# Kernel tuning notes

Measured on AMD Instinct MI355X. Metric: run time of the kernel, lower is better.

The kernel has to match this reference:

```python
import jax, jax.numpy as jnp
import numpy as np

N = 50000
E = 640000
D = 128
H = 512
LN_EPS = 1e-5


def setup_inputs() -> dict:
    key = jax.random.key(0)
    ks = jax.random.split(key, 6)
    x = jax.random.normal(ks[0], (N, D), dtype=jnp.float32)
    edge_index = jax.random.randint(ks[1], (2, E), 0, N, dtype=jnp.int64)
    edge_dist = jax.random.uniform(ks[2], (E,), dtype=jnp.float32)
    # true out-degrees of src so degree normalization is realistic
    degrees = jax.ops.segment_sum(jnp.ones((E,), jnp.float32), edge_index[0], num_segments=N)
    W1 = jax.random.normal(ks[3], (2 * D + 2, H), dtype=jnp.float32) * (1.0 / np.sqrt(2 * D + 2))
    b1 = jnp.zeros((H,), jnp.float32)
    W2 = jax.random.normal(ks[4], (H, D), dtype=jnp.float32) * (1.0 / np.sqrt(H))
    b2 = jnp.zeros((D,), jnp.float32)
    gamma = jnp.ones((D,), jnp.float32)
    beta = jnp.zeros((D,), jnp.float32)
    return {"x": x, "W1": W1, "b1": b1, "W2": W2, "b2": b2,
            "gamma": gamma, "beta": beta,
            "edge_index": edge_index, "edge_dist": edge_dist, "degrees": degrees}


def reference(x, W1, b1, W2, b2, gamma, beta, edge_index, edge_dist, degrees):
    n = x.shape[0]
    src, dst = edge_index[0], edge_index[1]
    # gather neighbor features, scatter-add into source nodes
    msg = x[dst]                                             # [E, D]
    agg = jax.ops.segment_sum(msg, src, num_segments=n)      # [N, D]
    deg = jnp.maximum(degrees, 1.0)                          # clamp_min(1.0)
    agg = agg / deg[:, None]
    dist_sum = jax.ops.segment_sum(edge_dist, src, num_segments=n)  # [N]
    mean_dist = dist_sum / deg                               # [N]
    feat = jnp.concatenate([x, agg, degrees[:, None], mean_dist[:, None]], axis=-1)  # [N, 2D+2]
    h = jax.nn.relu(feat @ W1 + b1)
    out = h @ W2 + b2
    y = x + out
    mu = jnp.mean(y, axis=-1, keepdims=True)
    var = jnp.var(y, axis=-1, keepdims=True)
    return (y - mu) / jnp.sqrt(var + LN_EPS) * gamma + beta
```

## Files before the change

### kernel.cpp

```cpp
#include <hip/hip_runtime.h>
#include <hip/hip_bf16.h>

#define NN 50000
#define EE 640000
#define LN_EPS 1e-5f
#define KD 272
#define KB 544

typedef __bf16 bf16x8 __attribute__((ext_vector_type(8)));
typedef float f32x16 __attribute__((ext_vector_type(16)));

static __device__ __forceinline__ unsigned short f2bf(float f) {
    return __builtin_bit_cast(unsigned short, (__bf16)f);
}
static __device__ __forceinline__ float bflo(unsigned int u) {
    return __builtin_bit_cast(float, u << 16);
}
static __device__ __forceinline__ float bfhi(unsigned int u) {
    return __builtin_bit_cast(float, u & 0xffff0000u);
}

__global__ __launch_bounds__(256) void cast_x(const float* __restrict__ x,
                                              unsigned short* __restrict__ xbf) {
    int i = blockIdx.x * 256 + threadIdx.x;
    const float4* s = (const float4*)x + (size_t)i * 2;
    float4 a = s[0], b = s[1];
    unsigned short o[8] = { f2bf(a.x), f2bf(a.y), f2bf(a.z), f2bf(a.w),
                            f2bf(b.x), f2bf(b.y), f2bf(b.z), f2bf(b.w) };
    *(uint4*)(xbf + (size_t)i * 8) = *(const uint4*)o;
}

__global__ __launch_bounds__(256) void prep_weights(const float* __restrict__ W1,
                                                    const float* __restrict__ b1,
                                                    const float* __restrict__ W2,
                                                    unsigned short* __restrict__ W1Te,
                                                    unsigned short* __restrict__ W2T) {
    int b = blockIdx.x, tid = threadIdx.x;
    if (b < 512) {
        W1Te[(size_t)b * KD + tid] = f2bf(W1[(size_t)tid * 512 + b]);
        if (tid < 16) {
            float v = 0.f;
            if (tid == 0) v = W1[256 * 512 + b];
            else if (tid == 1) v = W1[257 * 512 + b];
            else if (tid == 2) v = b1[b];
            W1Te[(size_t)b * KD + 256 + tid] = f2bf(v);
        }
    } else {
        int c = b - 512;
        W2T[(size_t)c * 512 + tid]       = f2bf(W2[(size_t)tid * 128 + c]);
        W2T[(size_t)c * 512 + 256 + tid] = f2bf(W2[(size_t)(256 + tid) * 128 + c]);
    }
}

__global__ __launch_bounds__(256) void scanA(const float* __restrict__ degrees,
                                             int* __restrict__ blocksum) {
    __shared__ int wsum[4];
    int i = blockIdx.x * 256 + threadIdx.x;
    int v = (i < NN) ? (int)(degrees[i] + 0.5f) : 0;
    int s = v;
    for (int d = 1; d < 64; d <<= 1) s += __shfl_xor(s, d, 64);
    if ((threadIdx.x & 63) == 0) wsum[threadIdx.x >> 6] = s;
    __syncthreads();
    if (threadIdx.x == 0) blocksum[blockIdx.x] = wsum[0] + wsum[1] + wsum[2] + wsum[3];
}

__global__ __launch_bounds__(256) void scanB(const int* __restrict__ blocksum,
                                             int* __restrict__ blockoff, int nb) {
    __shared__ int wsum[4];
    int tid = threadIdx.x;
    int v = (tid < nb) ? blocksum[tid] : 0;
    int lane = tid & 63, wid = tid >> 6;
    int inc = v;
    for (int d = 1; d < 64; d <<= 1) { int t = __shfl_up(inc, d, 64); if (lane >= d) inc += t; }
    if (lane == 63) wsum[wid] = inc;
    __syncthreads();
    int add = 0;
    for (int w = 0; w < wid; w++) add += wsum[w];
    inc += add;
    if (tid < nb) blockoff[tid] = inc - v;
}

__global__ __launch_bounds__(256) void scanC(const float* __restrict__ degrees,
                                             const int* __restrict__ blockoff,
                                             int* __restrict__ start,
                                             int* __restrict__ cursor) {
    __shared__ int wsum[4];
    int tid = threadIdx.x;
    int i = blockIdx.x * 256 + tid;
    int v = (i < NN) ? (int)(degrees[i] + 0.5f) : 0;
    int lane = tid & 63, wid = tid >> 6;
    int inc = v;
    for (int d = 1; d < 64; d <<= 1) { int t = __shfl_up(inc, d, 64); if (lane >= d) inc += t; }
    if (lane == 63) wsum[wid] = inc;
    __syncthreads();
    int add = blockoff[blockIdx.x];
    for (int w = 0; w < wid; w++) add += wsum[w];
    int excl = add + inc - v;
    if (i < NN) { start[i] = excl; cursor[i] = excl; }
}

__global__ __launch_bounds__(256) void sort_kernel(const int* __restrict__ ei,
                                                   const float* __restrict__ edist,
                                                   int* __restrict__ cursor,
                                                   int* __restrict__ sorted_dst,
                                                   float* __restrict__ dist_sum) {
    int e = blockIdx.x * 256 + threadIdx.x;
    if (e >= EE) return;
    int s = ei[e];
    int d = ei[EE + e];
    int p = atomicAdd(cursor + s, 1);
    sorted_dst[p] = d;
    atomicAdd(dist_sum + s, edist[e]);
}

__global__ __launch_bounds__(256) void aggfeat_kernel(const unsigned short* __restrict__ xbf,
                                                      const int* __restrict__ start,
                                                      const float* __restrict__ degrees,
                                                      const int* __restrict__ sorted_dst,
                                                      const float* __restrict__ dist,
                                                      unsigned short* __restrict__ featbf) {
    int tid = threadIdx.x;
    int node = blockIdx.x * 4 + (tid >> 6);
    int lane = tid & 63;
    if (node >= NN) return;
    int st = start[node];
    int cnt = (int)(degrees[node] + 0.5f);
    float a0 = 0.f, a1 = 0.f;
    for (int base = 0; base < cnt; base += 64) {
        int rem = cnt - base;
        int nv = rem < 64 ? rem : 64;
        int didx = (lane < nv) ? sorted_dst[st + base + lane] : 0;
        int j = 0;
        for (; j + 4 <= nv; j += 4) {
            int d0 = __shfl(didx, j,     64);
            int d1 = __shfl(didx, j + 1, 64);
            int d2 = __shfl(didx, j + 2, 64);
            int d3 = __shfl(didx, j + 3, 64);
            unsigned int v0 = *(const unsigned int*)(xbf + (size_t)d0 * 128 + lane * 2);
            unsigned int v1 = *(const unsigned int*)(xbf + (size_t)d1 * 128 + lane * 2);
            unsigned int v2 = *(const unsigned int*)(xbf + (size_t)d2 * 128 + lane * 2);
            unsigned int v3 = *(const unsigned int*)(xbf + (size_t)d3 * 128 + lane * 2);
            a0 += bflo(v0) + bflo(v1) + bflo(v2) + bflo(v3);
            a1 += bfhi(v0) + bfhi(v1) + bfhi(v2) + bfhi(v3);
        }
        for (; j < nv; j++) {
            int dj = __shfl(didx, j, 64);
            unsigned int v = *(const unsigned int*)(xbf + (size_t)dj * 128 + lane * 2);
            a0 += bflo(v);
            a1 += bfhi(v);
        }
    }
    float degc = fmaxf(degrees[node], 1.0f);
    float inv = 1.0f / degc;
    unsigned short* row = featbf + (size_t)node * KD;
    *(unsigned int*)(row + lane * 2) = *(const unsigned int*)(xbf + (size_t)node * 128 + lane * 2);
    unsigned short o2[2] = { f2bf(a0 * inv), f2bf(a1 * inv) };
    *(unsigned int*)(row + 128 + lane * 2) = *(const unsigned int*)o2;
    if (lane < 4) {
        unsigned short t4[4] = { 0, 0, 0, 0 };
        if (lane == 0) { t4[0] = f2bf(degrees[node]); t4[1] = f2bf(dist[node] * inv); t4[2] = f2bf(1.0f); }
        *(uint2*)(row + 256 + lane * 4) = *(const uint2*)t4;
    }
}

__global__ __launch_bounds__(256, 2) void fused_mlp_ln(const unsigned short* __restrict__ featbf,
                                                       const unsigned short* __restrict__ W1Te,
                                                       const unsigned short* __restrict__ W2T,
                                                       const float* __restrict__ x,
                                                       const float* __restrict__ b2,
                                                       const float* __restrict__ gamma,
                                                       const float* __restrict__ beta,
                                                       float* __restrict__ out) {
    __shared__ __align__(16) unsigned char lds[34816 + 16384];
    unsigned char* B1 = lds;
    unsigned char* B2 = lds + 34816;

    int tid = threadIdx.x;
    int wave = tid >> 6, lane = tid & 63;
    int ln = lane & 31, hi = lane >> 5;
    int rowbase = blockIdx.x * 128 + wave * 32;
    int gr = rowbase + ln;
    int xorv = (ln & 7) << 4;

    bf16x8 ffr[17];
    if (gr < NN) {
        const unsigned char* fp = (const unsigned char*)featbf + (size_t)gr * KB + hi * 16;
#pragma unroll
        for (int ks = 0; ks < 17; ks++)
            ffr[ks] = *(const bf16x8*)(fp + ks * 32);
    } else {
#pragma unroll
        for (int ks = 0; ks < 17; ks++) ffr[ks] = (bf16x8)(__bf16)0.0f;
    }

    f32x16 acc2[4] = {};

    for (int ct = 0; ct < 8; ct++) {
        const unsigned short* s1 = W1Te + (size_t)(ct * 64) * KD;
        for (int i = tid; i < 2048; i += 256) {
            int c = i >> 5, slot = i & 31;
            uint4 v = *(const uint4*)(s1 + c * KD + slot * 8);
            *(uint4*)(B1 + ((c * KB + slot * 16) ^ ((c & 7) << 4))) = v;
        }
        if (tid < 128) {
            int c = tid >> 1, half = tid & 1;
            uint4 v = *(const uint4*)(s1 + c * KD + 256 + half * 8);
            *(uint4*)(B1 + ((c * KB + 512 + half * 16) ^ ((c & 7) << 4))) = v;
        }
        const unsigned short* s2 = W2T + ct * 64;
        for (int i = tid; i < 1024; i += 256) {
            int c = i >> 3, s = i & 7;
            uint4 v = *(const uint4*)(s2 + (size_t)c * 512 + s * 8);
            *(uint4*)(B2 + ((c * 128 + s * 16) ^ ((c & 7) << 4))) = v;
        }
        __syncthreads();

        f32x16 acc1[2] = {};
#pragma unroll
        for (int ks = 0; ks < 17; ks++) {
#pragma unroll
            for (int t = 0; t < 2; t++) {
                int col = t * 32 + ln;
                bf16x8 af = *(const bf16x8*)(B1 + ((col * KB + ks * 32 + hi * 16) ^ xorv));
                acc1[t] = __builtin_amdgcn_mfma_f32_32x32x16_bf16(af, ffr[ks], acc1[t], 0, 0, 0);
            }
        }

        unsigned int dw[2][4][2];
#pragma unroll
        for (int t = 0; t < 2; t++)
#pragma unroll
            for (int g = 0; g < 4; g++)
#pragma unroll
                for (int i = 0; i < 2; i++) {
                    float lo = fmaxf(acc1[t][g * 4 + 2 * i], 0.f);
                    float hf = fmaxf(acc1[t][g * 4 + 2 * i + 1], 0.f);
                    dw[t][g][i] = (unsigned int)f2bf(lo) | ((unsigned int)f2bf(hf) << 16);
                }

#pragma unroll
        for (int t = 0; t < 2; t++)
#pragma unroll
            for (int w = 0; w < 2; w++) {
                int ks2 = t * 2 + w;
                unsigned int sL0 = dw[t][2 * w][0],     sL1 = dw[t][2 * w][1];
                unsigned int sH0 = dw[t][2 * w + 1][0], sH1 = dw[t][2 * w + 1][1];
                unsigned int send0 = hi ? sL0 : sH0;
                unsigned int send1 = hi ? sL1 : sH1;
                unsigned int r0 = (unsigned int)__shfl_xor((int)send0, 32, 64);
                unsigned int r1 = (unsigned int)__shfl_xor((int)send1, 32, 64);
                uint4 fd;
                fd.x = hi ? r0 : sL0;
                fd.y = hi ? r1 : sL1;
                fd.z = hi ? sH0 : r0;
                fd.w = hi ? sH1 : r1;
                bf16x8 hfr = __builtin_bit_cast(bf16x8, fd);
#pragma unroll
                for (int at = 0; at < 4; at++) {
                    int col2 = at * 32 + ln;
                    bf16x8 a2 = *(const bf16x8*)(B2 + ((col2 * 128 + ks2 * 32 + hi * 16) ^ xorv));
                    acc2[at] = __builtin_amdgcn_mfma_f32_32x32x16_bf16(a2, hfr, acc2[at], 0, 0, 0);
                }
            }
        __syncthreads();
    }

    bool rok = (gr < NN);
    float sum = 0.f, sq = 0.f;
#pragma unroll
    for (int at = 0; at < 4; at++)
#pragma unroll
        for (int g = 0; g < 4; g++) {
            int c0 = at * 32 + g * 8 + hi * 4;
            float4 bq = *(const float4*)(b2 + c0);
            float4 xq = rok ? *(const float4*)(x + (size_t)gr * 128 + c0) : make_float4(0, 0, 0, 0);
            float vb[4] = { bq.x, bq.y, bq.z, bq.w };
            float vx[4] = { xq.x, xq.y, xq.z, xq.w };
#pragma unroll
            for (int m = 0; m < 4; m++) {
                float v = acc2[at][g * 4 + m] + vb[m] + vx[m];
                acc2[at][g * 4 + m] = v;
                sum += v;
                sq += v * v;
            }
        }
    sum += __shfl_xor(sum, 32, 64);
    sq  += __shfl_xor(sq, 32, 64);
    float mu = sum * (1.0f / 128.0f);
    float var = sq * (1.0f / 128.0f) - mu * mu;
    float rs = rsqrtf(var + LN_EPS);
    if (rok) {
        float* orow = out + (size_t)gr * 128;
#pragma unroll
        for (int at = 0; at < 4; at++)
#pragma unroll
            for (int g = 0; g < 4; g++) {
                int c0 = at * 32 + g * 8 + hi * 4;
                float4 gq = *(const float4*)(gamma + c0);
                float4 be = *(const float4*)(beta + c0);
                float4 o;
                o.x = (acc2[at][g * 4 + 0] - mu) * rs * gq.x + be.x;
                o.y = (acc2[at][g * 4 + 1] - mu) * rs * gq.y + be.y;
                o.z = (acc2[at][g * 4 + 2] - mu) * rs * gq.z + be.z;
                o.w = (acc2[at][g * 4 + 3] - mu) * rs * gq.w + be.w;
                *(float4*)(orow + c0) = o;
            }
    }
}

extern "C" void kernel_launch(void* const* d_in, const int* in_sizes, int n_in,
                              void* d_out, int out_size, void* d_ws, size_t ws_size,
                              hipStream_t stream) {
    const float* x       = (const float*)d_in[0];
    const float* W1      = (const float*)d_in[1];
    const float* b1      = (const float*)d_in[2];
    const float* W2      = (const float*)d_in[3];
    const float* b2      = (const float*)d_in[4];
    const float* gamma   = (const float*)d_in[5];
    const float* beta    = (const float*)d_in[6];
    const int*   ei      = (const int*)d_in[7];
    const float* edist   = (const float*)d_in[8];
    const float* degrees = (const float*)d_in[9];
    float* out = (float*)d_out;

    char* ws = (char*)d_ws;
    size_t off = 0;
    auto alloc = [&](size_t bytes) {
        void* p = ws + off;
        off = (off + bytes + 255) & ~(size_t)255;
        return p;
    };
    int* sorted_dst         = (int*)alloc((size_t)EE * 4);
    int* startA             = (int*)alloc((size_t)NN * 4);
    int* cursor             = (int*)alloc((size_t)NN * 4);
    float* dist             = (float*)alloc((size_t)NN * 4);
    int* blocksum           = (int*)alloc(256 * 4);
    int* blockoff           = (int*)alloc(256 * 4);
    unsigned short* xbf     = (unsigned short*)alloc((size_t)NN * 128 * 2);
    unsigned short* featbf  = (unsigned short*)alloc((size_t)NN * KD * 2);
    unsigned short* W1Te    = (unsigned short*)alloc((size_t)512 * KD * 2);
    unsigned short* W2T     = (unsigned short*)alloc((size_t)128 * 512 * 2);

    const int NB = (NN + 255) / 256;

    hipMemsetAsync(dist, 0, (size_t)NN * 4, stream);
    cast_x<<<3125, 256, 0, stream>>>(x, xbf);
    prep_weights<<<640, 256, 0, stream>>>(W1, b1, W2, W1Te, W2T);
    scanA<<<NB, 256, 0, stream>>>(degrees, blocksum);
    scanB<<<1, 256, 0, stream>>>(blocksum, blockoff, NB);
    scanC<<<NB, 256, 0, stream>>>(degrees, blockoff, startA, cursor);
    sort_kernel<<<(EE + 255) / 256, 256, 0, stream>>>(ei, edist, cursor, sorted_dst, dist);
    aggfeat_kernel<<<(NN + 3) / 4, 256, 0, stream>>>(xbf, startA, degrees, sorted_dst, dist, featbf);
    fused_mlp_ln<<<(NN + 127) / 128, 256, 0, stream>>>(featbf, W1Te, W2T, x, b2, gamma, beta, out);
}
```

Before: 253.8 us.

## Replace per-node counting sort with bucketed binning and LDS-atomic aggregation

Swaps the per-node exclusive scan plus global-atomic scatter sort for a coarse sort into buckets of 128 source nodes. Each block stages its edges in LDS, then writes them to global memory as packed records holding dst, local src and bf16 distance. Aggregation then runs per half-bucket with LDS float atomics into a 64x128 accumulator, so per-node start offsets and global dist atomics are no longer needed. The intent is to cut global atomic contention and launch count. In exchange, every record is read twice (once per half-block), LDS atomics add contention, and edge distance drops to bf16 precision.

```diff
diff --git a/kernel.cpp b/kernel.cpp
--- a/kernel.cpp
+++ b/kernel.cpp
@@ -6,6 +6,8 @@
 #define LN_EPS 1e-5f
 #define KD 272
 #define KB 544
+#define NBK 391
+#define CH 4096
 
 typedef __bf16 bf16x8 __attribute__((ext_vector_type(8)));
 typedef float f32x16 __attribute__((ext_vector_type(16)));
@@ -52,114 +54,174 @@
     }
 }
 
-__global__ __launch_bounds__(256) void scanA(const float* __restrict__ degrees,
-                                             int* __restrict__ blocksum) {
-    __shared__ int wsum[4];
-    int i = blockIdx.x * 256 + threadIdx.x;
+__global__ __launch_bounds__(128) void hist_kernel(const float* __restrict__ degrees,
+                                                   int* __restrict__ bcnt) {
+    __shared__ int ws[2];
+    int tid = threadIdx.x, lane = tid & 63, wid = tid >> 6;
+    int i = blockIdx.x * 128 + tid;
     int v = (i < NN) ? (int)(degrees[i] + 0.5f) : 0;
     int s = v;
     for (int d = 1; d < 64; d <<= 1) s += __shfl_xor(s, d, 64);
-    if ((threadIdx.x & 63) == 0) wsum[threadIdx.x >> 6] = s;
-    __syncthreads();
-    if (threadIdx.x == 0) blocksum[blockIdx.x] = wsum[0] + wsum[1] + wsum[2] + wsum[3];
-}
-
-__global__ __launch_bounds__(256) void scanB(const int* __restrict__ blocksum,
-                                             int* __restrict__ blockoff, int nb) {
+    if (lane == 0) ws[wid] = s;
+    __syncthreads();
+    if (tid == 0) bcnt[blockIdx.x] = ws[0] + ws[1];
+}
+
+__global__ __launch_bounds__(256) void scan_buckets(const int* __restrict__ bcnt,
+                                                    int* __restrict__ gbase,
+                                                    int* __restrict__ gcur) {
     __shared__ int wsum[4];
-    int tid = threadIdx.x;
-    int v = (tid < nb) ? blocksum[tid] : 0;
-    int lane = tid & 63, wid = tid >> 6;
-    int inc = v;
+    int tid = threadIdx.x, lane = tid & 63, wid = tid >> 6;
+    int t2 = tid * 2;
+    int v0 = (t2 < NBK) ? bcnt[t2] : 0;
+    int v1 = (t2 + 1 < NBK) ? bcnt[t2 + 1] : 0;
+    int s2 = v0 + v1;
+    int inc = s2;
     for (int d = 1; d < 64; d <<= 1) { int t = __shfl_up(inc, d, 64); if (lane >= d) inc += t; }
     if (lane == 63) wsum[wid] = inc;
     __syncthreads();
-    int add = 0;
-    for (int w = 0; w < wid; w++) add += wsum[w];
-    inc += add;
-    if (tid < nb) blockoff[tid] = inc - v;
-}
-
-__global__ __launch_bounds__(256) void scanC(const float* __restrict__ degrees,
-                                             const int* __restrict__ blockoff,
-                                             int* __restrict__ start,
-                                             int* __restrict__ cursor) {
+    int base = 0;
+    for (int w = 0; w < wid; w++) base += wsum[w];
+    int ep = base + inc - s2;
+    if (t2 < NBK)     { gbase[t2] = ep;      gcur[t2] = ep; }
+    if (t2 + 1 < NBK) { gbase[t2 + 1] = ep + v0; gcur[t2 + 1] = ep + v0; }
+}
+
+__global__ __launch_bounds__(256) void bin_kernel(const int* __restrict__ ei,
+                                                  const float* __restrict__ edist,
+                                                  int* __restrict__ gcur,
+                                                  uint2* __restrict__ recs) {
+    __shared__ int cnt[NBK], off[NBK], gb[NBK], c2[NBK];
     __shared__ int wsum[4];
-    int tid = threadIdx.x;
-    int i = blockIdx.x * 256 + tid;
-    int v = (i < NN) ? (int)(degrees[i] + 0.5f) : 0;
-    int lane = tid & 63, wid = tid >> 6;
-    int inc = v;
-    for (int d = 1; d < 64; d <<= 1) { int t = __shfl_up(inc, d, 64); if (lane >= d) inc += t; }
-    if (lane == 63) wsum[wid] = inc;
-    __syncthreads();
-    int add = blockoff[blockIdx.x];
-    for (int w = 0; w < wid; w++) add += wsum[w];
-    int excl = add + inc - v;
-    if (i < NN) { start[i] = excl; cursor[i] = excl; }
-}
-
-__global__ __launch_bounds__(256) void sort_kernel(const int* __restrict__ ei,
-                                                   const float* __restrict__ edist,
-                                                   int* __restrict__ cursor,
-                                                   int* __restrict__ sorted_dst,
-                                                   float* __restrict__ dist_sum) {
-    int e = blockIdx.x * 256 + threadIdx.x;
-    if (e >= EE) return;
-    int s = ei[e];
-    int d = ei[EE + e];
-    int p = atomicAdd(cursor + s, 1);
-    sorted_dst[p] = d;
-    atomicAdd(dist_sum + s, edist[e]);
-}
-
-__global__ __launch_bounds__(256) void aggfeat_kernel(const unsigned short* __restrict__ xbf,
-                                                      const int* __restrict__ start,
-                                                      const float* __restrict__ degrees,
-                                                      const int* __restrict__ sorted_dst,
-                                                      const float* __restrict__ dist,
-                                                      unsigned short* __restrict__ featbf) {
-    int tid = threadIdx.x;
-    int node = blockIdx.x * 4 + (tid >> 6);
-    int lane = tid & 63;
+    __shared__ uint2 stage[CH];
+    __shared__ int gtg[CH];
+    int tid = threadIdx.x, lane = tid & 63, wid = tid >> 6;
+    int e0 = blockIdx.x * CH;
+    int nval = EE - e0; if (nval > CH) nval = CH;
+
+    for (int i = tid; i < NBK; i += 256) { cnt[i] = 0; c2[i] = 0; }
+    __syncthreads();
+#pragma unroll
+    for (int k = 0; k < CH / 256; k++) {
+        int e = e0 + k * 256 + tid;
+        if (e < EE) atomicAdd(&cnt[ei[e] >> 7], 1);
+    }
+    __syncthreads();
+    {
+        int t2 = tid * 2;
+        int v0 = (t2 < NBK) ? cnt[t2] : 0;
+        int v1 = (t2 + 1 < NBK) ? cnt[t2 + 1] : 0;
+        int s2 = v0 + v1;
+        int inc = s2;
+        for (int d = 1; d < 64; d <<= 1) { int t = __shfl_up(inc, d, 64); if (lane >= d) inc += t; }
+        if (lane == 63) wsum[wid] = inc;
+        __syncthreads();
+        int base = 0;
+        for (int w = 0; w < wid; w++) base += wsum[w];
+        int ep = base + inc - s2;
+        if (t2 < NBK)     off[t2] = ep;
+        if (t2 + 1 < NBK) off[t2 + 1] = ep + v0;
+    }
+    __syncthreads();
+    for (int i = tid; i < NBK; i += 256) {
+        int c = cnt[i];
+        gb[i] = c ? atomicAdd(&gcur[i], c) : 0;
+    }
+    __syncthreads();
+#pragma unroll
+    for (int k = 0; k < CH / 256; k++) {
+        int e = e0 + k * 256 + tid;
+        if (e < EE) {
+            int s = ei[e];
+            int d = ei[EE + e];
+            float dv = edist[e];
+            int b = s >> 7;
+            int p = atomicAdd(&c2[b], 1);
+            int slot = off[b] + p;
+            stage[slot] = make_uint2((unsigned)d, ((unsigned)(s & 127) << 16) | f2bf(dv));
+            gtg[slot] = gb[b] + p;
+        }
+    }
+    __syncthreads();
+    for (int i = tid; i < nval; i += 256)
+        recs[gtg[i]] = stage[i];
+}
+
+__global__ __launch_bounds__(256) void aggbucket_kernel(const unsigned short* __restrict__ xbf,
+                                                        const uint2* __restrict__ recs,
+                                                        const int* __restrict__ gbase,
+                                                        const int* __restrict__ bcnt,
+                                                        const float* __restrict__ degrees,
+                                                        unsigned short* __restrict__ featbf) {
+    __shared__ float agg[64][128];
+    __shared__ float dl[64];
+    int tid = threadIdx.x, wave = tid >> 6, lane = tid & 63;
+    int bkt = blockIdx.x >> 1, half = blockIdx.x & 1;
+    int st = gbase[bkt], cnt = bcnt[bkt];
+
+    for (int k = tid; k < 64 * 128; k += 256) ((float*)agg)[k] = 0.f;
+    if (tid < 64) dl[tid] = 0.f;
+    __syncthreads();
+
+    for (int i = wave * 2; i < cnt; i += 8) {
+        uint2 rA = recs[st + i];
+        bool hasB = (i + 1) < cnt;
+        uint2 rB = hasB ? recs[st + i + 1] : make_uint2(0u, 0u);
+        unsigned sA = rA.y >> 16, sB = rB.y >> 16;
+        bool doA = (sA >> 6) == (unsigned)half;
+        bool doB = hasB && ((sB >> 6) == (unsigned)half);
+        unsigned xvA = 0, xvB = 0;
+        if (doA) xvA = *(const unsigned*)(xbf + (size_t)rA.x * 128 + lane * 2);
+        if (doB) xvB = *(const unsigned*)(xbf + (size_t)rB.x * 128 + lane * 2);
+        if (doA) {
+            int r = sA & 63;
+            atomicAdd(&agg[r][lane], bflo(xvA));
+            atomicAdd(&agg[r][64 + lane], bfhi(xvA));
+            if (lane == 0) atomicAdd(&dl[r], bflo(rA.y));
+        }
+        if (doB) {
+            int r = sB & 63;
+            atomicAdd(&agg[r][lane], bflo(xvB));
+            atomicAdd(&agg[r][64 + lane], bfhi(xvB));
+            if (lane == 0) atomicAdd(&dl[r], bflo(rB.y));
+        }
+    }
+    __syncthreads();
+
+    int r = tid >> 2, seg = tid & 3;
+    int node = bkt * 128 + half * 64 + r;
     if (node >= NN) return;
-    int st = start[node];
-    int cnt = (int)(degrees[node] + 0.5f);
-    float a0 = 0.f, a1 = 0.f;
-    for (int base = 0; base < cnt; base += 64) {
-        int rem = cnt - base;
-        int nv = rem < 64 ? rem : 64;
-        int didx = (lane < nv) ? sorted_dst[st + base + lane] : 0;
-        int j = 0;
-        for (; j + 4 <= nv; j += 4) {
-            int d0 = __shfl(didx, j,     64);
-            int d1 = __shfl(didx, j + 1, 64);
-            int d2 = __shfl(didx, j + 2, 64);
-            int d3 = __shfl(didx, j + 3, 64);
-            unsigned int v0 = *(const unsigned int*)(xbf + (size_t)d0 * 128 + lane * 2);
-            unsigned int v1 = *(const unsigned int*)(xbf + (size_t)d1 * 128 + lane * 2);
-            unsigned int v2 = *(const unsigned int*)(xbf + (size_t)d2 * 128 + lane * 2);
-            unsigned int v3 = *(const unsigned int*)(xbf + (size_t)d3 * 128 + lane * 2);
-            a0 += bflo(v0) + bflo(v1) + bflo(v2) + bflo(v3);
-            a1 += bfhi(v0) + bfhi(v1) + bfhi(v2) + bfhi(v3);
-        }
-        for (; j < nv; j++) {
-            int dj = __shfl(didx, j, 64);
-            unsigned int v = *(const unsigned int*)(xbf + (size_t)dj * 128 + lane * 2);
-            a0 += bflo(v);
-            a1 += bfhi(v);
-        }
-    }
-    float degc = fmaxf(degrees[node], 1.0f);
+    float dg = degrees[node];
+    float degc = fmaxf(dg, 1.0f);
     float inv = 1.0f / degc;
     unsigned short* row = featbf + (size_t)node * KD;
-    *(unsigned int*)(row + lane * 2) = *(const unsigned int*)(xbf + (size_t)node * 128 + lane * 2);
-    unsigned short o2[2] = { f2bf(a0 * inv), f2bf(a1 * inv) };
-    *(unsigned int*)(row + 128 + lane * 2) = *(const unsigned int*)o2;
-    if (lane < 4) {
-        unsigned short t4[4] = { 0, 0, 0, 0 };
-        if (lane == 0) { t4[0] = f2bf(degrees[node]); t4[1] = f2bf(dist[node] * inv); t4[2] = f2bf(1.0f); }
-        *(uint2*)(row + 256 + lane * 4) = *(const uint2*)t4;
+    const unsigned short* xr = xbf + (size_t)node * 128 + seg * 32;
+    uint4 sa = *(const uint4*)(xr);
+    uint4 sb = *(const uint4*)(xr + 8);
+    uint4 sc = *(const uint4*)(xr + 16);
+    uint4 sd = *(const uint4*)(xr + 24);
+    *(uint4*)(row + seg * 32)      = sa;
+    *(uint4*)(row + seg * 32 + 8)  = sb;
+    *(uint4*)(row + seg * 32 + 16) = sc;
+    *(uint4*)(row + seg * 32 + 24) = sd;
+    unsigned short o[32];
+#pragma unroll
+    for (int k = 0; k < 32; k++) {
+        int c = seg * 32 + k;
+        float v = agg[r][((c & 1) << 6) + (c >> 1)] * inv;
+        o[k] = f2bf(v);
+    }
+    *(uint4*)(row + 128 + seg * 32)      = *(const uint4*)(o);
+    *(uint4*)(row + 128 + seg * 32 + 8)  = *(const uint4*)(o + 8);
+    *(uint4*)(row + 128 + seg * 32 + 16) = *(const uint4*)(o + 16);
+    *(uint4*)(row + 128 + seg * 32 + 24) = *(const uint4*)(o + 24);
+    if (seg == 3) {
+        unsigned short t[16] = {0};
+        t[0] = f2bf(dg);
+        t[1] = f2bf(dl[r] * inv);
+        t[2] = f2bf(1.0f);
+        *(uint4*)(row + 256)     = *(const uint4*)(t);
+        *(uint4*)(row + 256 + 8) = *(const uint4*)(t + 8);
     }
 }
 
@@ -330,26 +392,20 @@
         off = (off + bytes + 255) & ~(size_t)255;
         return p;
     };
-    int* sorted_dst         = (int*)alloc((size_t)EE * 4);
-    int* startA             = (int*)alloc((size_t)NN * 4);
-    int* cursor             = (int*)alloc((size_t)NN * 4);
-    float* dist             = (float*)alloc((size_t)NN * 4);
-    int* blocksum           = (int*)alloc(256 * 4);
-    int* blockoff           = (int*)alloc(256 * 4);
+    uint2* recs             = (uint2*)alloc((size_t)EE * 8);
+    int* bcnt               = (int*)alloc(NBK * 4);
+    int* gbase              = (int*)alloc(NBK * 4);
+    int* gcur               = (int*)alloc(NBK * 4);
     unsigned short* xbf     = (unsigned short*)alloc((size_t)NN * 128 * 2);
     unsigned short* featbf  = (unsigned short*)alloc((size_t)NN * KD * 2);
     unsigned short* W1Te    = (unsigned short*)alloc((size_t)512 * KD * 2);
     unsigned short* W2T     = (unsigned short*)alloc((size_t)128 * 512 * 2);
 
-    const int NB = (NN + 255) / 256;
-
-    hipMemsetAsync(dist, 0, (size_t)NN * 4, stream);
     cast_x<<<3125, 256, 0, stream>>>(x, xbf);
     prep_weights<<<640, 256, 0, stream>>>(W1, b1, W2, W1Te, W2T);
-    scanA<<<NB, 256, 0, stream>>>(degrees, blocksum);
-    scanB<<<1, 256, 0, stream>>>(blocksum, blockoff, NB);
-    scanC<<<NB, 256, 0, stream>>>(degrees, blockoff, startA, cursor);
-    sort_kernel<<<(EE + 255) / 256, 256, 0, stream>>>(ei, edist, cursor, sorted_dst, dist);
-    aggfeat_kernel<<<(NN + 3) / 4, 256, 0, stream>>>(xbf, startA, degrees, sorted_dst, dist, featbf);
+    hist_kernel<<<NBK, 128, 0, stream>>>(degrees, bcnt);
+    scan_buckets<<<1, 256, 0, stream>>>(bcnt, gbase, gcur);
+    bin_kernel<<<(EE + CH - 1) / CH, 256, 0, stream>>>(ei, edist, gcur, recs);
+    aggbucket_kernel<<<NBK * 2, 256, 0, stream>>>(xbf, recs, gbase, bcnt, degrees, featbf);
     fused_mlp_ln<<<(NN + 127) / 128, 256, 0, stream>>>(featbf, W1Te, W2T, x, b2, gamma, beta, out);
 }
```

After: 731.0 us. 188% more time.

## Replace global-atomic edge sort with two-level LDS bucket sort

Applied to the files above, without the earlier changes.

The per-edge global atomic counting sort is replaced by two passes. First, blocks of 4096 edges are binned into 64-node buckets using LDS atomics, and each bucket reserves a global range with one atomic. Then a per-bucket kernel scatters records to their final node positions using LDS cursors. Destination indices are packed into 16-bit values, which shrinks the sorted index stream read by aggregation. This adds a kernel launch and relies on N fitting in 16 bits; the bin pass also runs only about 157 blocks.

```diff
diff --git a/kernel.cpp b/kernel.cpp
--- a/kernel.cpp
+++ b/kernel.cpp
@@ -6,6 +6,8 @@
 #define LN_EPS 1e-5f
 #define KD 272
 #define KB 544
+#define NBK2 782
+#define CH 4096
 
 typedef __bf16 bf16x8 __attribute__((ext_vector_type(8)));
 typedef float f32x16 __attribute__((ext_vector_type(16)));
@@ -83,7 +85,7 @@
 __global__ __launch_bounds__(256) void scanC(const float* __restrict__ degrees,
                                              const int* __restrict__ blockoff,
                                              int* __restrict__ start,
-                                             int* __restrict__ cursor) {
+                                             int* __restrict__ gcur) {
     __shared__ int wsum[4];
     int tid = threadIdx.x;
     int i = blockIdx.x * 256 + tid;
@@ -96,27 +98,103 @@
     int add = blockoff[blockIdx.x];
     for (int w = 0; w < wid; w++) add += wsum[w];
     int excl = add + inc - v;
-    if (i < NN) { start[i] = excl; cursor[i] = excl; }
-}
-
-__global__ __launch_bounds__(256) void sort_kernel(const int* __restrict__ ei,
-                                                   const float* __restrict__ edist,
-                                                   int* __restrict__ cursor,
-                                                   int* __restrict__ sorted_dst,
-                                                   float* __restrict__ dist_sum) {
-    int e = blockIdx.x * 256 + threadIdx.x;
-    if (e >= EE) return;
-    int s = ei[e];
-    int d = ei[EE + e];
-    int p = atomicAdd(cursor + s, 1);
-    sorted_dst[p] = d;
-    atomicAdd(dist_sum + s, edist[e]);
+    if (i < NN) {
+        start[i] = excl;
+        if ((i & 63) == 0) gcur[i >> 6] = excl;
+    }
+}
+
+__global__ __launch_bounds__(256) void bin_kernel(const int* __restrict__ ei,
+                                                  const float* __restrict__ edist,
+                                                  int* __restrict__ gcur,
+                                                  unsigned* __restrict__ recs1,
+                                                  float* __restrict__ dist) {
+    __shared__ int cnt[NBK2], off[NBK2], gb[NBK2], c2[NBK2];
+    __shared__ int wsum[4];
+    __shared__ unsigned stage[CH];
+    __shared__ int gtg[CH];
+    int tid = threadIdx.x, lane = tid & 63, wid = tid >> 6;
+    int e0 = blockIdx.x * CH;
+    int nval = EE - e0; if (nval > CH) nval = CH;
+
+    for (int i = tid; i < NBK2; i += 256) { cnt[i] = 0; c2[i] = 0; }
+    __syncthreads();
+#pragma unroll
+    for (int k = 0; k < CH / 256; k++) {
+        int e = e0 + k * 256 + tid;
+        if (e < EE) atomicAdd(&cnt[ei[e] >> 6], 1);
+    }
+    __syncthreads();
+    {
+        int v[4], s = 0;
+#pragma unroll
+        for (int j = 0; j < 4; j++) {
+            int idx = tid * 4 + j;
+            v[j] = (idx < NBK2) ? cnt[idx] : 0;
+            s += v[j];
+        }
+        int inc = s;
+        for (int d = 1; d < 64; d <<= 1) { int t = __shfl_up(inc, d, 64); if (lane >= d) inc += t; }
+        if (lane == 63) wsum[wid] = inc;
+        __syncthreads();
+        int base = 0;
+        for (int w = 0; w < wid; w++) base += wsum[w];
+        int ex = base + inc - s;
+#pragma unroll
+        for (int j = 0; j < 4; j++) {
+            int idx = tid * 4 + j;
+            if (idx < NBK2) off[idx] = ex;
+            ex += v[j];
+        }
+    }
+    __syncthreads();
+    for (int i = tid; i < NBK2; i += 256) {
+        int c = cnt[i];
+        gb[i] = c ? atomicAdd(&gcur[i], c) : 0;
+    }
+    __syncthreads();
+#pragma unroll
+    for (int k = 0; k < CH / 256; k++) {
+        int e = e0 + k * 256 + tid;
+        if (e < EE) {
+            int s = ei[e];
+            int d = ei[EE + e];
+            atomicAdd(dist + s, edist[e]);
+            int b = s >> 6;
+            int p = atomicAdd(&c2[b], 1);
+            int slot = off[b] + p;
+            stage[slot] = (unsigned)d | ((unsigned)(s & 63) << 16);
+            gtg[slot] = gb[b] + p;
+        }
+    }
+    __syncthreads();
+    for (int i = tid; i < nval; i += 256)
+        recs1[gtg[i]] = stage[i];
+}
+
+__global__ __launch_bounds__(256) void subsort_kernel(const unsigned* __restrict__ recs1,
+                                                      const int* __restrict__ start,
+                                                      unsigned short* __restrict__ recs2) {
+    __shared__ int cur[64];
+    int bkt = blockIdx.x, tid = threadIdx.x;
+    int bstart = start[bkt * 64];
+    int bend = (bkt == NBK2 - 1) ? EE : start[(bkt + 1) * 64];
+    if (tid < 64) {
+        int node = bkt * 64 + tid;
+        cur[tid] = (node < NN) ? start[node] : EE;
+    }
+    __syncthreads();
+    for (int i = bstart + tid; i < bend; i += 256) {
+        unsigned r = recs1[i];
+        int p = atomicAdd(&cur[(r >> 16) & 63], 1);
+        recs2[p] = (unsigned short)(r & 0xffffu);
+    }
 }
 
 __global__ __launch_bounds__(256) void aggfeat_kernel(const unsigned short* __restrict__ xbf,
                                                       const int* __restrict__ start,
                                                       const float* __restrict__ degrees,
-                                                      const int* __restrict__ sorted_dst,
+                                                      const unsigned short* __restrict__ recs2,
                                                       const float* __restrict__ dist,
                                                       unsigned short* __restrict__ featbf) {
     int tid = threadIdx.x;
@@ -129,28 +207,29 @@
     for (int base = 0; base < cnt; base += 64) {
         int rem = cnt - base;
         int nv = rem < 64 ? rem : 64;
-        int didx = (lane < nv) ? sorted_dst[st + base + lane] : 0;
+        int didx = (lane < nv) ? (int)recs2[st + base + lane] : 0;
         int j = 0;
         for (; j + 4 <= nv; j += 4) {
             int d0 = __shfl(didx, j,     64);
             int d1 = __shfl(didx, j + 1, 64);
             int d2 = __shfl(didx, j + 2, 64);
             int d3 = __shfl(didx, j + 3, 64);
-            unsigned int v0 = *(const unsigned int*)(xbf + (size_t)d0 * 128 + lane * 2);
-            unsigned int v1 = *(const unsigned int*)(xbf + (size_t)d1 * 128 + lane * 2);
-            unsigned int v2 = *(const unsigned int*)(xbf + (size_t)d2 * 128 + lane * 2);
-            unsigned int v3 = *(const unsigned int*)(xbf + (size_t)d3 * 128 + lane * 2);
-            a0 += bflo(v0) + bflo(v1) + bflo(v2) + bflo(v3);
-            a1 += bfhi(v0) + bfhi(v1) + bfhi(v2) + bfhi(v3);
+            unsigned x0 = *(const unsigned*)(xbf + (size_t)d0 * 128 + lane * 2);
+            unsigned x1 = *(const unsigned*)(xbf + (size_t)d1 * 128 + lane * 2);
+            unsigned x2 = *(const unsigned*)(xbf + (size_t)d2 * 128 + lane * 2);
+            unsigned x3 = *(const unsigned*)(xbf + (size_t)d3 * 128 + lane * 2);
+            a0 += bflo(x0) + bflo(x1) + bflo(x2) + bflo(x3);
+            a1 += bfhi(x0) + bfhi(x1) + bfhi(x2) + bfhi(x3);
         }
         for (; j < nv; j++) {
             int dj = __shfl(didx, j, 64);
-            unsigned int v = *(const unsigned int*)(xbf + (size_t)dj * 128 + lane * 2);
-            a0 += bflo(v);
-            a1 += bfhi(v);
-        }
-    }
-    float degc = fmaxf(degrees[node], 1.0f);
+            unsigned xv = *(const unsigned*)(xbf + (size_t)dj * 128 + lane * 2);
+            a0 += bflo(xv);
+            a1 += bfhi(xv);
+        }
+    }
+    float dg = degrees[node];
+    float degc = fmaxf(dg, 1.0f);
     float inv = 1.0f / degc;
     unsigned short* row = featbf + (size_t)node * KD;
     *(unsigned int*)(row + lane * 2) = *(const unsigned int*)(xbf + (size_t)node * 128 + lane * 2);
@@ -158,7 +237,7 @@
     *(unsigned int*)(row + 128 + lane * 2) = *(const unsigned int*)o2;
     if (lane < 4) {
         unsigned short t4[4] = { 0, 0, 0, 0 };
-        if (lane == 0) { t4[0] = f2bf(degrees[node]); t4[1] = f2bf(dist[node] * inv); t4[2] = f2bf(1.0f); }
+        if (lane == 0) { t4[0] = f2bf(dg); t4[1] = f2bf(dist[node] * inv); t4[2] = f2bf(1.0f); }
         *(uint2*)(row + 256 + lane * 4) = *(const uint2*)t4;
     }
 }
@@ -330,12 +409,13 @@
         off = (off + bytes + 255) & ~(size_t)255;
         return p;
     };
-    int* sorted_dst         = (int*)alloc((size_t)EE * 4);
-    int* startA             = (int*)alloc((size_t)NN * 4);
-    int* cursor             = (int*)alloc((size_t)NN * 4);
-    float* dist             = (float*)alloc((size_t)NN * 4);
+    unsigned* recs1         = (unsigned*)alloc((size_t)EE * 4);
+    unsigned short* recs2   = (unsigned short*)alloc((size_t)EE * 2);
+    int* start              = (int*)alloc((size_t)NN * 4);
+    int* gcur               = (int*)alloc(NBK2 * 4);
     int* blocksum           = (int*)alloc(256 * 4);
     int* blockoff           = (int*)alloc(256 * 4);
+    float* dist             = (float*)alloc((size_t)NN * 4);
     unsigned short* xbf     = (unsigned short*)alloc((size_t)NN * 128 * 2);
     unsigned short* featbf  = (unsigned short*)alloc((size_t)NN * KD * 2);
     unsigned short* W1Te    = (unsigned short*)alloc((size_t)512 * KD * 2);
@@ -348,8 +428,9 @@
     prep_weights<<<640, 256, 0, stream>>>(W1, b1, W2, W1Te, W2T);
     scanA<<<NB, 256, 0, stream>>>(degrees, blocksum);
     scanB<<<1, 256, 0, stream>>>(blocksum, blockoff, NB);
-    scanC<<<NB, 256, 0, stream>>>(degrees, blockoff, startA, cursor);
-    sort_kernel<<<(EE + 255) / 256, 256, 0, stream>>>(ei, edist, cursor, sorted_dst, dist);
-    aggfeat_kernel<<<(NN + 3) / 4, 256, 0, stream>>>(xbf, startA, degrees, sorted_dst, dist, featbf);
+    scanC<<<NB, 256, 0, stream>>>(degrees, blockoff, start, gcur);
+    bin_kernel<<<(EE + CH - 1) / CH, 256, 0, stream>>>(ei, edist, gcur, recs1, dist);
+    subsort_kernel<<<NBK2, 256, 0, stream>>>(recs1, start, recs2);
+    aggfeat_kernel<<<(NN + 3) / 4, 256, 0, stream>>>(xbf, start, degrees, recs2, dist, featbf);
     fused_mlp_ln<<<(NN + 127) / 128, 256, 0, stream>>>(featbf, W1Te, W2T, x, b2, gamma, beta, out);
 }
```

New measurement: 238.0 us. 1.07x faster.
